# Kernel optimization log

Hardware: AMD Instinct MI355X
Metric: run time of the kernel (lower is better)

## Reference

```python
import jax, jax.numpy as jnp
import numpy as np

DIM = 1024
FF = 4096
E = 8
K = 2


def setup_inputs() -> dict:
    key = jax.random.key(0)
    ks = jax.random.split(key, 6)
    x = jax.random.normal(ks[0], (4, 2048, DIM), dtype=jnp.float32)
    wr = jax.random.normal(ks[1], (E, DIM), dtype=jnp.float32) * 0.02   # router weight [E, D]
    w1 = jax.random.normal(ks[2], (E, DIM, 2 * FF), dtype=jnp.float32) * 0.02  # SwiGLU in-proj
    b1 = jax.random.normal(ks[3], (E, 2 * FF), dtype=jnp.float32) * 0.02
    w2 = jax.random.normal(ks[4], (E, FF, DIM), dtype=jnp.float32) * 0.02  # SwiGLU out-proj
    b2 = jax.random.normal(ks[5], (E, DIM), dtype=jnp.float32) * 0.02
    return {"x": x, "wr": wr, "w1": w1, "b1": b1, "w2": w2, "b2": b2}


def reference(x, wr, w1, b1, w2, b2):
    B, T, D = x.shape
    n_experts = wr.shape[0]
    xf = x.reshape(B * T, D)                      # [N, D]
    logits = xf @ wr.T                            # [N, E]
    topk_vals, topk_idx = jax.lax.top_k(logits, K)  # [N, K]
    gates = jax.nn.softmax(topk_vals, axis=-1)      # [N, K]
    out = jnp.zeros_like(xf)
    for e in range(n_experts):
        # combined gate weight for tokens routed to expert e (0 otherwise)
        g_e = jnp.sum(jnp.where(topk_idx == e, gates, 0.0), axis=-1)  # [N]
        u = xf @ w1[e] + b1[e]                    # [N, 2F]
        a, b = jnp.split(u, 2, axis=-1)
        h = jax.nn.silu(a) * b                    # SwiGLU
        y_e = h @ w2[e] + b2[e]                   # [N, D]
        out = out + g_e[:, None] * y_e
    return out.reshape(B, T, D)
```

## Files before the change

kernel.cpp:

```cpp
#include <hip/hip_runtime.h>

#define NE 8
#define NTOK 8192
#define NDIM 1024
#define NFF 4096

typedef short bf16x8 __attribute__((ext_vector_type(8)));
typedef float f32x4 __attribute__((ext_vector_type(4)));
typedef unsigned short us_t;
typedef us_t us4 __attribute__((ext_vector_type(4)));

#define MFMA16 __builtin_amdgcn_mfma_f32_16x16x32_bf16

__device__ __forceinline__ us_t f2bf(float f) {
  unsigned int u = __float_as_uint(f);
  u += 0x7fffu + ((u >> 16) & 1u);
  return (us_t)(u >> 16);
}

__device__ __forceinline__ void gload16(const void* g, void* l) {
  __builtin_amdgcn_global_load_lds(
      (const __attribute__((address_space(1))) void*)g,
      (__attribute__((address_space(3))) void*)l, 16, 0, 0);
}

__global__ __launch_bounds__(256) void router_kernel(
    const float* __restrict__ x, const float* __restrict__ wr,
    int* __restrict__ counts, int* __restrict__ tok_list,
    int4* __restrict__ tok4, float2* __restrict__ gate2,
    us_t* __restrict__ xbf)
{
  __shared__ float wr_s[NE * NDIM];
  int tid = threadIdx.x;
#pragma unroll
  for (int i = 0; i < 8; ++i)
    ((float4*)wr_s)[tid + 256 * i] = ((const float4*)wr)[tid + 256 * i];
  __syncthreads();
  int w = tid >> 6, l = tid & 63;
  int t = blockIdx.x * 4 + w;
  float4 xv[4];
#pragma unroll
  for (int j = 0; j < 4; ++j) xv[j] = ((const float4*)x)[(size_t)t * 256 + j * 64 + l];
#pragma unroll
  for (int j = 0; j < 4; ++j) {
    us4 o;
    o.x = f2bf(xv[j].x); o.y = f2bf(xv[j].y); o.z = f2bf(xv[j].z); o.w = f2bf(xv[j].w);
    ((us4*)xbf)[(size_t)t * 256 + j * 64 + l] = o;
  }
  float logits[NE];
#pragma unroll
  for (int e = 0; e < NE; ++e) {
    float p = 0.f;
#pragma unroll
    for (int j = 0; j < 4; ++j) {
      float4 wv = ((const float4*)wr_s)[e * 256 + j * 64 + l];
      p += xv[j].x * wv.x + xv[j].y * wv.y + xv[j].z * wv.z + xv[j].w * wv.w;
    }
#pragma unroll
    for (int s = 32; s > 0; s >>= 1) p += __shfl_xor(p, s, 64);
    logits[e] = p;
  }
  if (l == 0) {
    int e1 = 0; float v1 = logits[0];
#pragma unroll
    for (int e = 1; e < NE; ++e) if (logits[e] > v1) { v1 = logits[e]; e1 = e; }
    int e2 = -1; float v2 = -3.4e38f;
#pragma unroll
    for (int e = 0; e < NE; ++e) if (e != e1 && logits[e] > v2) { v2 = logits[e]; e2 = e; }
    float ge = expf(v2 - v1);
    float g1 = 1.f / (1.f + ge);
    float g2 = 1.f - g1;
    int i1 = atomicAdd(&counts[e1], 1);
    tok_list[e1 * NTOK + i1] = t;
    int i2 = atomicAdd(&counts[e2], 1);
    tok_list[e2 * NTOK + i2] = t;
    tok4[t] = make_int4(e1, i1, e2, i2);
    gate2[t] = make_float2(g1, g2);
  }
}

__global__ void prefix8(const int* __restrict__ counts, int* __restrict__ offsets) {
  if (threadIdx.x == 0) {
    int s = 0;
    for (int e = 0; e < NE; ++e) { offsets[e] = s; s += counts[e]; }
  }
}

__global__ __launch_bounds__(256) void transpose_cvt(
    const float* __restrict__ in, us_t* __restrict__ out, int R, int C)
{
  __shared__ float tile[64][65];
  int e = blockIdx.z;
  const float* ip = in + (size_t)e * R * C;
  us_t* op = out + (size_t)e * R * C;
  int r0 = blockIdx.y * 64, c0 = blockIdx.x * 64;
  int tid = threadIdx.x;
#pragma unroll
  for (int q = 0; q < 4; ++q) {
    int id = tid + 256 * q;
    int rr = id >> 4, c4 = id & 15;
    float4 v = *(const float4*)&ip[(size_t)(r0 + rr) * C + c0 + c4 * 4];
    tile[rr][c4 * 4 + 0] = v.x; tile[rr][c4 * 4 + 1] = v.y;
    tile[rr][c4 * 4 + 2] = v.z; tile[rr][c4 * 4 + 3] = v.w;
  }
  __syncthreads();
#pragma unroll
  for (int q = 0; q < 4; ++q) {
    int id = tid + 256 * q;
    int cc = id >> 4, r4 = id & 15;
    us4 o;
    o.x = f2bf(tile[r4 * 4 + 0][cc]);
    o.y = f2bf(tile[r4 * 4 + 1][cc]);
    o.z = f2bf(tile[r4 * 4 + 2][cc]);
    o.w = f2bf(tile[r4 * 4 + 3][cc]);
    *(us4*)&op[(size_t)(c0 + cc) * R + r0 + r4 * 4] = o;
  }
}

__global__ __launch_bounds__(256) void gemm1_swiglu(
    const us_t* __restrict__ xbf,
    const us_t* __restrict__ w1T,
    const float* __restrict__ b1,
    const int* __restrict__ counts, const int* __restrict__ offsets,
    const int* __restrict__ tok_list,
    us_t* __restrict__ hbuf)
{
  const int e = blockIdx.z, mt = blockIdx.y, ct = blockIdx.x;
  const int cnt = counts[e];
  if (mt * 128 >= cnt) return;
  const int off = offsets[e];
  const int tid = threadIdx.x, w = tid >> 6, l = tid & 63;
  const int wr_ = w >> 1, wc = w & 1;

  __shared__ char ldsA[16384];
  __shared__ char ldsB[32768];
  __shared__ int tok_l[128];

  if (tid < 128) {
    int r = mt * 128 + tid;
    tok_l[tid] = tok_list[e * NTOK + (r < cnt ? r : cnt - 1)];
  }
  __syncthreads();

  unsigned int soff[12];
#pragma unroll
  for (int i = 0; i < 12; ++i) {
    int c = w + i * 4;
    if (i < 4) {
      int p = c * 1024 + l * 16;
      int row = p >> 7;
      int ir = (p & 127) ^ ((row & 7) << 4);
      soff[i] = (unsigned int)(tok_l[row] * 2048 + ir);
    } else {
      int cb = c - 16;
      int p = cb * 1024 + l * 16;
      int row = p >> 7;
      int ir = (p & 127) ^ ((row & 7) << 4);
      int ncol = (row < 128) ? (ct * 128 + row) : (NFF + ct * 128 + (row - 128));
      soff[i] = (unsigned int)(ncol * 2048 + ir);
    }
  }

  f32x4 zf = {0.f, 0.f, 0.f, 0.f};
  f32x4 acc[2][4][4];
#pragma unroll
  for (int h_ = 0; h_ < 2; ++h_)
#pragma unroll
    for (int cg = 0; cg < 4; ++cg)
#pragma unroll
      for (int rg = 0; rg < 4; ++rg) acc[h_][cg][rg] = zf;

  const char* xB = (const char*)xbf;
  const char* wB = (const char*)w1T + (size_t)e * (2 * NFF) * NDIM * 2;

  for (int ktb = 0; ktb < NDIM * 2; ktb += 128) {
    __syncthreads();
#pragma unroll
    for (int i = 0; i < 4; ++i)
      gload16(xB + soff[i] + ktb, ldsA + (w + i * 4) * 1024);
#pragma unroll
    for (int i = 4; i < 12; ++i)
      gload16(wB + soff[i] + ktb, ldsB + (w + i * 4 - 16) * 1024);
    __syncthreads();
#pragma unroll
    for (int ks = 0; ks < 2; ++ks) {
      bf16x8 af[4];
#pragma unroll
      for (int rg = 0; rg < 4; ++rg) {
        int row = wr_ * 64 + rg * 16 + (l & 15);
        int ir = (ks * 64 + (l >> 4) * 16) ^ ((row & 7) << 4);
        af[rg] = *(const bf16x8*)(ldsA + row * 128 + ir);
      }
#pragma unroll
      for (int h_ = 0; h_ < 2; ++h_)
#pragma unroll
        for (int cg = 0; cg < 4; ++cg) {
          int crow = h_ * 128 + wc * 64 + cg * 16 + (l & 15);
          int ir = (ks * 64 + (l >> 4) * 16) ^ ((crow & 7) << 4);
          bf16x8 bfr = *(const bf16x8*)(ldsB + crow * 128 + ir);
#pragma unroll
          for (int rg = 0; rg < 4; ++rg)
            acc[h_][cg][rg] = MFMA16(af[rg], bfr, acc[h_][cg][rg], 0, 0, 0);
        }
    }
  }

  float b1a[4], b1b[4];
#pragma unroll
  for (int cg = 0; cg < 4; ++cg) {
    int n_a = ct * 128 + wc * 64 + cg * 16 + (l & 15);
    b1a[cg] = b1[e * 2 * NFF + n_a];
    b1b[cg] = b1[e * 2 * NFF + NFF + n_a];
  }
#pragma unroll
  for (int cg = 0; cg < 4; ++cg) {
    int n_a = ct * 128 + wc * 64 + cg * 16 + (l & 15);
#pragma unroll
    for (int rg = 0; rg < 4; ++rg) {
#pragma unroll
      for (int j = 0; j < 4; ++j) {
        int rt = wr_ * 64 + rg * 16 + (l >> 4) * 4 + j;
        int r = mt * 128 + rt;
        if (r < cnt) {
          float a = acc[0][cg][rg][j] + b1a[cg];
          float b = acc[1][cg][rg][j] + b1b[cg];
          float hv = (a / (1.f + __expf(-a))) * b;
          hbuf[(size_t)(off + r) * NFF + n_a] = f2bf(hv);
        }
      }
    }
  }
}

__global__ __launch_bounds__(256) void gemm2_slot(
    const us_t* __restrict__ hbuf,
    const us_t* __restrict__ w2T,
    const float* __restrict__ b2,
    const int* __restrict__ counts, const int* __restrict__ offsets,
    float* __restrict__ ybuf)
{
  const int e = blockIdx.z, mt = blockIdx.y, nt = blockIdx.x;
  const int cnt = counts[e];
  if (mt * 128 >= cnt) return;
  const int off = offsets[e];
  const int tid = threadIdx.x, w = tid >> 6, l = tid & 63;
  const int wr_ = w >> 1, wc = w & 1;

  __shared__ char ldsA[16384];
  __shared__ char ldsB[16384];

  unsigned int soff[8];
#pragma unroll
  for (int i = 0; i < 8; ++i) {
    int c = w + i * 4;
    if (i < 4) {
      int p = c * 1024 + l * 16;
      int row = p >> 7;
      int ir = (p & 127) ^ ((row & 7) << 4);
      int r = mt * 128 + row; if (r >= cnt) r = cnt - 1;
      soff[i] = (unsigned int)((off + r) * (NFF * 2) + ir);
    } else {
      int cb = c - 16;
      int p = cb * 1024 + l * 16;
      int row = p >> 7;
      int ir = (p & 127) ^ ((row & 7) << 4);
      soff[i] = (unsigned int)((nt * 128 + row) * (NFF * 2) + ir);
    }
  }

  f32x4 zf = {0.f, 0.f, 0.f, 0.f};
  f32x4 acc[4][4];
#pragma unroll
  for (int cg = 0; cg < 4; ++cg)
#pragma unroll
    for (int rg = 0; rg < 4; ++rg) acc[cg][rg] = zf;

  const char* hB = (const char*)hbuf;
  const char* wB = (const char*)w2T + (size_t)e * NDIM * NFF * 2;

  for (int ktb = 0; ktb < NFF * 2; ktb += 128) {
    __syncthreads();
#pragma unroll
    for (int i = 0; i < 4; ++i)
      gload16(hB + soff[i] + ktb, ldsA + (w + i * 4) * 1024);
#pragma unroll
    for (int i = 4; i < 8; ++i)
      gload16(wB + soff[i] + ktb, ldsB + (w + i * 4 - 16) * 1024);
    __syncthreads();
#pragma unroll
    for (int ks = 0; ks < 2; ++ks) {
      bf16x8 af[4];
#pragma unroll
      for (int rg = 0; rg < 4; ++rg) {
        int row = wr_ * 64 + rg * 16 + (l & 15);
        int ir = (ks * 64 + (l >> 4) * 16) ^ ((row & 7) << 4);
        af[rg] = *(const bf16x8*)(ldsA + row * 128 + ir);
      }
#pragma unroll
      for (int cg = 0; cg < 4; ++cg) {
        int crow = wc * 64 + cg * 16 + (l & 15);
        int ir = (ks * 64 + (l >> 4) * 16) ^ ((crow & 7) << 4);
        bf16x8 bfr = *(const bf16x8*)(ldsB + crow * 128 + ir);
#pragma unroll
        for (int rg = 0; rg < 4; ++rg)
          acc[cg][rg] = MFMA16(af[rg], bfr, acc[cg][rg], 0, 0, 0);
      }
    }
  }

#pragma unroll
  for (int cg = 0; cg < 4; ++cg) {
    int col = nt * 128 + wc * 64 + cg * 16 + (l & 15);
    float b2v = b2[e * NDIM + col];
#pragma unroll
    for (int rg = 0; rg < 4; ++rg) {
#pragma unroll
      for (int j = 0; j < 4; ++j) {
        int rt = wr_ * 64 + rg * 16 + (l >> 4) * 4 + j;
        int r = mt * 128 + rt;
        if (r < cnt)
          ybuf[(size_t)(off + r) * NDIM + col] = acc[cg][rg][j] + b2v;
      }
    }
  }
}

__global__ __launch_bounds__(256) void combine_kernel(
    const float* __restrict__ ybuf, const int* __restrict__ offsets,
    const int4* __restrict__ tok4, const float2* __restrict__ gate2,
    float* __restrict__ out)
{
  int t = blockIdx.x;
  int4 p = tok4[t];
  float2 g = gate2[t];
  int s1 = offsets[p.x] + p.y;
  int s2 = offsets[p.z] + p.w;
  const float4* y1 = (const float4*)(ybuf + (size_t)s1 * NDIM);
  const float4* y2 = (const float4*)(ybuf + (size_t)s2 * NDIM);
  float4 a = y1[threadIdx.x];
  float4 b = y2[threadIdx.x];
  float4 o;
  o.x = g.x * a.x + g.y * b.x;
  o.y = g.x * a.y + g.y * b.y;
  o.z = g.x * a.z + g.y * b.z;
  o.w = g.x * a.w + g.y * b.w;
  ((float4*)(out + (size_t)t * NDIM))[threadIdx.x] = o;
}

extern "C" void kernel_launch(void* const* d_in, const int* in_sizes, int n_in,
                              void* d_out, int out_size, void* d_ws, size_t ws_size,
                              hipStream_t stream) {
  const float* x  = (const float*)d_in[0];
  const float* wr = (const float*)d_in[1];
  const float* w1 = (const float*)d_in[2];
  const float* b1 = (const float*)d_in[3];
  const float* w2 = (const float*)d_in[4];
  const float* b2 = (const float*)d_in[5];
  float* out = (float*)d_out;
  char* ws = (char*)d_ws;

  int*    counts   = (int*)(ws + 0);
  int*    offsets  = (int*)(ws + 256);
  int*    tok_list = (int*)(ws + 512);
  int4*   tok4     = (int4*)(ws + 512 + 262144);
  float2* gate2    = (float2*)(ws + 512 + 262144 + 131072);
  us_t*   xbf      = (us_t*)(ws + 524800);
  us_t*   hbuf     = (us_t*)(ws + 524800 + (size_t)NTOK * NDIM * 2);
  us_t*   wT       = (us_t*)(ws + 524800 + (size_t)NTOK * NDIM * 2
                                          + (size_t)2 * NTOK * NFF * 2);
  float*  ybuf     = (float*)((char*)wT + 67108864);

  hipMemsetAsync(counts, 0, 32, stream);

  router_kernel<<<NTOK / 4, 256, 0, stream>>>(x, wr, counts, tok_list, tok4, gate2, xbf);
  prefix8<<<1, 64, 0, stream>>>(counts, offsets);

  transpose_cvt<<<dim3(2 * NFF / 64, NDIM / 64, NE), 256, 0, stream>>>(w1, wT, NDIM, 2 * NFF);
  gemm1_swiglu<<<dim3(NFF / 128, NTOK / 128, NE), 256, 0, stream>>>(
      xbf, wT, b1, counts, offsets, tok_list, hbuf);

  transpose_cvt<<<dim3(NDIM / 64, NFF / 64, NE), 256, 0, stream>>>(w2, wT, NFF, NDIM);
  gemm2_slot<<<dim3(NDIM / 128, NTOK / 128, NE), 256, 0, stream>>>(
      hbuf, wT, b2, counts, offsets, ybuf);

  combine_kernel<<<NTOK, 256, 0, stream>>>(ybuf, offsets, tok4, gate2, out);
}
```

Measured before the change: 984.4 us.

## Remap GEMM block indices for XCD-aware L2 locality and widen transpose stores

Both expert GEMMs switch to a 1D grid whose block index is decoded so blocks landing on the same XCD share the same weight column tiles or token tiles, aiming to improve L2 reuse across the MI355X chiplets. gemm1 recomputes its global-load addresses inside the K loop instead of keeping 12 precomputed offsets in registers, which lowers register pressure but adds address arithmetic. The transpose-convert kernel writes 8 bf16 values per store instead of 4. The index decode hardcodes the grid shape, so it is tied to these exact problem sizes.

New measurement: 1.786 ms. 1.81x slower.

```diff
diff --git a/kernel.cpp b/kernel.cpp
--- a/kernel.cpp
+++ b/kernel.cpp
@@ -9,6 +9,7 @@
 typedef float f32x4 __attribute__((ext_vector_type(4)));
 typedef unsigned short us_t;
 typedef us_t us4 __attribute__((ext_vector_type(4)));
+typedef us_t us8 __attribute__((ext_vector_type(8)));
 
 #define MFMA16 __builtin_amdgcn_mfma_f32_16x16x32_bf16
 
@@ -105,15 +106,13 @@
   }
   __syncthreads();
 #pragma unroll
-  for (int q = 0; q < 4; ++q) {
+  for (int q = 0; q < 2; ++q) {
     int id = tid + 256 * q;
-    int cc = id >> 4, r4 = id & 15;
-    us4 o;
-    o.x = f2bf(tile[r4 * 4 + 0][cc]);
-    o.y = f2bf(tile[r4 * 4 + 1][cc]);
-    o.z = f2bf(tile[r4 * 4 + 2][cc]);
-    o.w = f2bf(tile[r4 * 4 + 3][cc]);
-    *(us4*)&op[(size_t)(c0 + cc) * R + r0 + r4 * 4] = o;
+    int cc = id >> 3, r8 = id & 7;
+    us8 o;
+#pragma unroll
+    for (int j = 0; j < 8; ++j) o[j] = f2bf(tile[r8 * 8 + j][cc]);
+    *(us8*)&op[(size_t)(c0 + cc) * R + r0 + r8 * 8] = o;
   }
 }
 
@@ -125,7 +124,12 @@
     const int* __restrict__ tok_list,
     us_t* __restrict__ hbuf)
 {
-  const int e = blockIdx.z, mt = blockIdx.y, ct = blockIdx.x;
+  const int b = blockIdx.x;
+  const int xcd = b & 7, k = b >> 3;
+  const int mt = xcd * 8 + (k & 7);
+  const int ct = (k >> 3) & 31;
+  const int e  = k >> 8;
+
   const int cnt = counts[e];
   if (mt * 128 >= cnt) return;
   const int off = offsets[e];
@@ -142,25 +146,6 @@
   }
   __syncthreads();
 
-  unsigned int soff[12];
-#pragma unroll
-  for (int i = 0; i < 12; ++i) {
-    int c = w + i * 4;
-    if (i < 4) {
-      int p = c * 1024 + l * 16;
-      int row = p >> 7;
-      int ir = (p & 127) ^ ((row & 7) << 4);
-      soff[i] = (unsigned int)(tok_l[row] * 2048 + ir);
-    } else {
-      int cb = c - 16;
-      int p = cb * 1024 + l * 16;
-      int row = p >> 7;
-      int ir = (p & 127) ^ ((row & 7) << 4);
-      int ncol = (row < 128) ? (ct * 128 + row) : (NFF + ct * 128 + (row - 128));
-      soff[i] = (unsigned int)(ncol * 2048 + ir);
-    }
-  }
-
   f32x4 zf = {0.f, 0.f, 0.f, 0.f};
   f32x4 acc[2][4][4];
 #pragma unroll
@@ -170,17 +155,31 @@
 #pragma unroll
       for (int rg = 0; rg < 4; ++rg) acc[h_][cg][rg] = zf;
 
-  const char* xB = (const char*)xbf;
-  const char* wB = (const char*)w1T + (size_t)e * (2 * NFF) * NDIM * 2;
-
-  for (int ktb = 0; ktb < NDIM * 2; ktb += 128) {
+  const size_t w1base = (size_t)e * 2 * NFF * NDIM;
+
+  for (int kt = 0; kt < NDIM; kt += 64) {
     __syncthreads();
 #pragma unroll
-    for (int i = 0; i < 4; ++i)
-      gload16(xB + soff[i] + ktb, ldsA + (w + i * 4) * 1024);
-#pragma unroll
-    for (int i = 4; i < 12; ++i)
-      gload16(wB + soff[i] + ktb, ldsB + (w + i * 4 - 16) * 1024);
+    for (int i = 0; i < 12; ++i) {
+      int c = w + i * 4;
+      const us_t* gsrc; char* ldst;
+      if (c < 16) {
+        int p = c * 1024 + l * 16;
+        int row = p >> 7;
+        int ir = (p & 127) ^ ((row & 7) << 4);
+        gsrc = xbf + (size_t)tok_l[row] * NDIM + kt + (ir >> 1);
+        ldst = ldsA + c * 1024;
+      } else {
+        int cb = c - 16;
+        int p = cb * 1024 + l * 16;
+        int row = p >> 7;
+        int ir = (p & 127) ^ ((row & 7) << 4);
+        int ncol = (row < 128) ? (ct * 128 + row) : (NFF + ct * 128 + row - 128);
+        gsrc = w1T + w1base + (size_t)ncol * NDIM + kt + (ir >> 1);
+        ldst = ldsB + cb * 1024;
+      }
+      gload16(gsrc, ldst);
+    }
     __syncthreads();
 #pragma unroll
     for (int ks = 0; ks < 2; ++ks) {
@@ -239,7 +238,12 @@
     const int* __restrict__ counts, const int* __restrict__ offsets,
     float* __restrict__ ybuf)
 {
-  const int e = blockIdx.z, mt = blockIdx.y, nt = blockIdx.x;
+  const int b = blockIdx.x;
+  const int xcd = b & 7, k = b >> 3;
+  const int mt = k & 63;
+  const int combo = xcd + 8 * (k >> 6);
+  const int nt = combo & 7, e = combo >> 3;
+
   const int cnt = counts[e];
   if (mt * 128 >= cnt) return;
   const int off = offsets[e];
@@ -376,11 +380,11 @@
   prefix8<<<1, 64, 0, stream>>>(counts, offsets);
 
   transpose_cvt<<<dim3(2 * NFF / 64, NDIM / 64, NE), 256, 0, stream>>>(w1, wT, NDIM, 2 * NFF);
-  gemm1_swiglu<<<dim3(NFF / 128, NTOK / 128, NE), 256, 0, stream>>>(
+  gemm1_swiglu<<<16384, 256, 0, stream>>>(
       xbf, wT, b1, counts, offsets, tok_list, hbuf);
 
   transpose_cvt<<<dim3(NDIM / 64, NFF / 64, NE), 256, 0, stream>>>(w2, wT, NFF, NDIM);
-  gemm2_slot<<<dim3(NDIM / 128, NTOK / 128, NE), 256, 0, stream>>>(
+  gemm2_slot<<<4096, 256, 0, stream>>>(
       hbuf, wT, b2, counts, offsets, ybuf);
 
   combine_kernel<<<NTOK, 256, 0, stream>>>(ybuf, offsets, tok4, gate2, out);
```
